# Performance work log

Measured on AMD Instinct MI355X. Metric: run time of the kernel, lower is better.

## Reference

```python
import jax, jax.numpy as jnp
import numpy as np

N = 20000   # nodes per graph batch
E = 160000  # edges
G = 128     # graphs in batch
F = 114     # node feature dim (num_features == num_features_xd)
H = 10      # GAT heads
HF = F * H  # 1140


def setup_inputs() -> dict:
    key = jax.random.key(0)
    ks = jax.random.split(key, 64)
    ki = iter(range(64))
    def rn(shape, scale=0.05):
        return jax.random.normal(ks[next(ki)], shape, dtype=jnp.float32) * scale
    inp = {}
    inp["x1"] = jax.random.normal(ks[next(ki)], (N, F), dtype=jnp.float32)
    inp["edge_index1"] = jax.random.randint(ks[next(ki)], (2, E), 0, N)
    inp["batch1"] = jnp.sort(jax.random.randint(ks[next(ki)], (N,), 0, G))
    inp["x2"] = jax.random.normal(ks[next(ki)], (N, F), dtype=jnp.float32)
    inp["edge_index2"] = jax.random.randint(ks[next(ki)], (2, E), 0, N)
    inp["batch2"] = jnp.sort(jax.random.randint(ks[next(ki)], (N,), 0, G))
    inp["target"] = jax.random.normal(ks[next(ki)], (G, 1000), dtype=jnp.float32)
    for p in ("p1", "p2"):
        inp[p + "_gatW"] = rn((F, HF))
        inp[p + "_att_src"] = rn((H, F))
        inp[p + "_att_dst"] = rn((H, F))
        inp[p + "_gatb"] = rn((HF,))
        inp[p + "_gcnW"] = rn((HF, HF))
        inp[p + "_gcnb"] = rn((HF,))
        inp[p + "_fcg1W"] = rn((2 * HF, 1000))
        inp[p + "_fcg1b"] = rn((1000,))
        inp[p + "_fcg2W"] = rn((1000, 64))
        inp[p + "_fcg2b"] = rn((64,))
    inp["fcxtW"] = rn((1000, 128)); inp["fcxtb"] = rn((128,))
    inp["fc1W"] = rn((256, 128)); inp["fc1b"] = rn((128,))
    inp["fc2W"] = rn((128, 32)); inp["fc2b"] = rn((32,))
    inp["outW"] = rn((32, 1)); inp["outb"] = rn((1,))
    return inp


def lrelu(v):
    return jax.nn.leaky_relu(v, 0.01)  # nn.LeakyReLU default slope


def gat_conv(x, src, dst, W, att_src, att_dst, b):
    # PyG GATConv (concat heads, add_self_loops handled by caller)
    h = (x @ W).reshape(N, H, F)                     # [N,H,F]
    a_s = jnp.sum(h * att_src[None], axis=-1)        # [N,H]
    a_d = jnp.sum(h * att_dst[None], axis=-1)        # [N,H]
    e = jax.nn.leaky_relu(a_s[src] + a_d[dst], 0.2)  # [E',H]
    m = jax.ops.segment_max(e, dst, num_segments=N)
    ex = jnp.exp(e - m[dst])
    den = jax.ops.segment_sum(ex, dst, num_segments=N)
    alpha = ex / den[dst]                            # softmax over incoming edges
    out = jax.ops.segment_sum(alpha[:, :, None] * h[src], dst, num_segments=N)
    return out.reshape(N, HF) + b


def gcn_conv(x, src, dst, W, b):
    # PyG GCNConv with self loops (added by caller), symmetric normalization
    deg = jax.ops.segment_sum(jnp.ones_like(dst, dtype=x.dtype), dst, num_segments=N)
    dinv = jax.lax.rsqrt(jnp.maximum(deg, 1.0))
    h = x @ W                                        # [N,HF]
    msg = (dinv[src] * dinv[dst])[:, None] * h[src]
    return jax.ops.segment_sum(msg, dst, num_segments=N) + b


def branch(x, edge_index, batch, gatW, a_s, a_d, gatb, gcnW, gcnb, f1W, f1b, f2W, f2b):
    loop = jnp.arange(N, dtype=edge_index.dtype)
    src = jnp.concatenate([edge_index[0], loop])
    dst = jnp.concatenate([edge_index[1], loop])
    h = lrelu(gat_conv(x, src, dst, gatW, a_s, a_d, gatb))
    h = lrelu(gcn_conv(h, src, dst, gcnW, gcnb))
    mx = jax.ops.segment_max(h, batch, num_segments=G)
    mx = jnp.where(jnp.isfinite(mx), mx, 0.0)        # guard empty graphs
    cnt = jax.ops.segment_sum(jnp.ones((N,), h.dtype), batch, num_segments=G)
    mean = jax.ops.segment_sum(h, batch, num_segments=G) / jnp.maximum(cnt, 1.0)[:, None]
    g = jnp.concatenate([mx, mean], axis=1)          # [G, 2*HF]
    g = lrelu(g @ f1W + f1b)                         # dropout is identity at eval
    return g @ f2W + f2b                             # [G, 64]


def reference(x1, edge_index1, batch1, x2, edge_index2, batch2, target,
              p1_gatW, p1_att_src, p1_att_dst, p1_gatb, p1_gcnW, p1_gcnb,
              p1_fcg1W, p1_fcg1b, p1_fcg2W, p1_fcg2b,
              p2_gatW, p2_att_src, p2_att_dst, p2_gatb, p2_gcnW, p2_gcnb,
              p2_fcg1W, p2_fcg1b, p2_fcg2W, p2_fcg2b,
              fcxtW, fcxtb, fc1W, fc1b, fc2W, fc2b, outW, outb):
    g1 = branch(x1, edge_index1, batch1, p1_gatW, p1_att_src, p1_att_dst, p1_gatb,
                p1_gcnW, p1_gcnb, p1_fcg1W, p1_fcg1b, p1_fcg2W, p1_fcg2b)
    g2 = branch(x2, edge_index2, batch2, p2_gatW, p2_att_src, p2_att_dst, p2_gatb,
                p2_gcnW, p2_gcnb, p2_fcg1W, p2_fcg1b, p2_fcg2W, p2_fcg2b)
    xd = jnp.concatenate([g1, g2], axis=1)           # [G,128]
    xt = target.reshape(-1, 1000) @ fcxtW + fcxtb    # [G,128]
    xc = jnp.concatenate([xd, xt], axis=1)           # [G,256]
    xc = lrelu(xc @ fc1W + fc1b)
    xc = lrelu(xc @ fc2W + fc2b)
    return xc @ outW + outb                          # [G,1]
```

## Files before the change

kernel.cpp:

```cpp
#include <hip/hip_runtime.h>
#include <cstddef>
#include <cstdint>

#define NN 20000
#define EE 160000
#define EPRIME 180000
#define GG 128
#define FF 114
#define HH 10
#define HFD 1140
#define KP 1152
#define F1K 2280
#define F1KS 18
#define F1KC 128
#define NSCB 79

typedef unsigned short ushort_t;
typedef __attribute__((ext_vector_type(8))) short bf16x8;
typedef __attribute__((ext_vector_type(4))) float f32x4;

static constexpr size_t REL  = (size_t)NN * KP;
static constexpr size_t ZREL = (size_t)10 * NN * 128;

static inline int cdiv(int a, int b) { return (a + b - 1) / b; }


__device__ __forceinline__ ushort_t f2bf(float v) {
    union { float f; unsigned u; } c; c.f = v;
    unsigned u = c.u;
    unsigned r = (u + 0x7fffu + ((u >> 16) & 1u)) >> 16;
    return (ushort_t)r;
}
__device__ __forceinline__ float bf2f(ushort_t h) {
    union { unsigned u; float f; } c; c.u = ((unsigned)h) << 16;
    return c.f;
}

__device__ __forceinline__ void gload16(const void* g, const ushort_t* l) {
    __builtin_amdgcn_global_load_lds(
        (const __attribute__((address_space(1))) unsigned int*)g,
        (__attribute__((address_space(3))) unsigned int*)l, 16, 0, 0);
}


__global__ void k_init(int* __restrict__ deg, int* __restrict__ gstart, int* __restrict__ gend) {
    int br = blockIdx.y;
    int i = blockIdx.x * blockDim.x + threadIdx.x;
    if (i < NN) deg[br * NN + i] = 1;
    if (i < GG) { gstart[br * GG + i] = NN; gend[br * GG + i] = 0; }
}

__global__ void k_count(const int* __restrict__ ei0, const int* __restrict__ ei1,
                        int* __restrict__ deg) {
    int br = blockIdx.y;
    const int* ei = br ? ei1 : ei0;
    int i = blockIdx.x * blockDim.x + threadIdx.x;
    if (i < EE) atomicAdd(&deg[br * NN + ei[EE + i]], 1);
}

__global__ void k_scan1(const int* __restrict__ deg, int* __restrict__ offs, int* __restrict__ bsum) {
    __shared__ int tmp[256];
    int br = blockIdx.y;
    deg += br * NN; offs += br * (NN + 1); bsum += br * 128;
    int b = blockIdx.x, tid = threadIdx.x;
    int i = b * 256 + tid;
    int v = (i < NN) ? deg[i] : 0;
    tmp[tid] = v;
    __syncthreads();
#pragma unroll
    for (int off = 1; off < 256; off <<= 1) {
        int t = (tid >= off) ? tmp[tid - off] : 0;
        __syncthreads();
        tmp[tid] += t;
        __syncthreads();
    }
    if (i < NN) offs[i + 1] = tmp[tid];
    if (tid == 255) bsum[b] = tmp[255];
}

__global__ void k_scan2(int* __restrict__ bsum) {
    __shared__ int tmp[128];
    bsum += blockIdx.y * 128;
    int tid = threadIdx.x;
    int v = (tid < NSCB) ? bsum[tid] : 0;
    tmp[tid] = v;
    __syncthreads();
#pragma unroll
    for (int off = 1; off < 128; off <<= 1) {
        int t = (tid >= off) ? tmp[tid - off] : 0;
        __syncthreads();
        tmp[tid] += t;
        __syncthreads();
    }
    if (tid < NSCB) bsum[tid] = tmp[tid] - v;
}

__global__ void k_scan3prep(int* __restrict__ offs, const int* __restrict__ bsum,
                            int* __restrict__ cursor, const int* __restrict__ deg,
                            float* __restrict__ dinv,
                            const int* __restrict__ batch0, const int* __restrict__ batch1,
                            int* __restrict__ gstart, int* __restrict__ gend) {
    int br = blockIdx.y;
    offs += br * (NN + 1); bsum += br * 128; cursor += br * NN;
    deg += br * NN; dinv += br * NN;
    const int* batch = br ? batch1 : batch0;
    gstart += br * GG; gend += br * GG;
    int i = blockIdx.x * 256 + threadIdx.x;
    if (i < NN) {
        int o = offs[i + 1] + bsum[i >> 8];
        offs[i + 1] = o;
        cursor[i] = o - deg[i];
        dinv[i] = rsqrtf((float)deg[i]);
        int b = batch[i];
        atomicMin(&gstart[b], i);
        atomicMax(&gend[b], i + 1);
    }
    if (i == 0) offs[0] = 0;
}

__global__ void k_fill(const int* __restrict__ ei0, const int* __restrict__ ei1,
                       int* __restrict__ cursor, int* __restrict__ csr) {
    int br = blockIdx.y;
    const int* ei = br ? ei1 : ei0;
    cursor += br * NN; csr += (size_t)br * EPRIME;
    int i = blockIdx.x * blockDim.x + threadIdx.x;
    if (i < EPRIME) {
        int s, d;
        if (i < EE) { s = ei[i]; d = ei[EE + i]; }
        else        { s = i - EE; d = s; }
        int pos = atomicAdd(&cursor[d], 1);
        csr[pos] = s;
    }
}


__global__ void k_split_x(const float* __restrict__ x0, const float* __restrict__ x1,
                          ushort_t* __restrict__ xb) {
    int br = blockIdx.y;
    const float* x = br ? x1 : x0;
    xb += (size_t)br * REL;
    int idx = blockIdx.x * 256 + threadIdx.x;
    if (idx >= NN * 128) return;
    int n = idx >> 7, k = idx & 127;
    float v = (k < FF) ? x[(size_t)n * FF + k] : 0.f;
    xb[idx] = f2bf(v);
}

__global__ __launch_bounds__(256) void k_tbf(const float* __restrict__ W0, const float* __restrict__ W1,
                                             int K, int Nc, int Kpad, ushort_t* __restrict__ T) {
    __shared__ float tile[64][65];
    int br = blockIdx.z;
    const float* W = br ? W1 : W0;
    T += (size_t)br * KP * KP;
    int kb = blockIdx.x * 64;
    int nb = blockIdx.y * 64;
    int c = threadIdx.x & 63, r4 = threadIdx.x >> 6;
#pragma unroll
    for (int rr = 0; rr < 16; ++rr) {
        int r = r4 * 16 + rr;
        int gk = kb + r, gn = nb + c;
        tile[r][c] = (gk < K && gn < Nc) ? W[(size_t)gk * Nc + gn] : 0.f;
    }
    __syncthreads();
#pragma unroll
    for (int rr = 0; rr < 16; ++rr) {
        int r = r4 * 16 + rr;
        int gn = nb + r, gk = kb + c;
        T[(size_t)gn * Kpad + gk] = f2bf(tile[c][r]);
    }
}

__global__ __launch_bounds__(256) void k_wgtT(const float* __restrict__ W0, const float* __restrict__ W1,
                                              ushort_t* __restrict__ WgT) {
    __shared__ float tile[64][65];
    int y = blockIdx.z;
    int br = y / 10, h = y - 10 * br;
    const float* W = br ? W1 : W0;
    ushort_t* T = WgT + ((size_t)br * 10 + h) * 128 * 128;
    int kb = blockIdx.x * 64, cb = blockIdx.y * 64;
    int c = threadIdx.x & 63, r4 = threadIdx.x >> 6;
#pragma unroll
    for (int rr = 0; rr < 16; ++rr) {
        int r = r4 * 16 + rr;
        int gk = kb + r, gc = cb + c;
        tile[r][c] = (gk < FF && gc < FF) ? W[(size_t)gk * HFD + h * FF + gc] : 0.f;
    }
    __syncthreads();
#pragma unroll
    for (int rr = 0; rr < 16; ++rr) {
        int r = r4 * 16 + rr;
        int gc2 = cb + r, gk2 = kb + c;
        T[(size_t)gc2 * 128 + gk2] = f2bf(tile[c][r]);
    }
}

__global__ void k_vsd(const float* __restrict__ W0, const float* __restrict__ W1,
                      const float* __restrict__ as0, const float* __restrict__ as1,
                      const float* __restrict__ ad0, const float* __restrict__ ad1,
                      float* __restrict__ Vs, float* __restrict__ Vd) {
    int br = blockIdx.y;
    const float* W = br ? W1 : W0;
    const float* asrc = br ? as1 : as0;
    const float* adst = br ? ad1 : ad0;
    int idx = blockIdx.x * 256 + threadIdx.x;
    if (idx >= 1280) return;
    int k = idx / 10, h = idx - 10 * (idx / 10);
    float vs = 0.f, vd = 0.f;
    if (k < FF) {
        const float* wrow = W + (size_t)k * HFD + h * FF;
        const float* s = asrc + h * FF;
        const float* d = adst + h * FF;
        for (int f = 0; f < FF; ++f) { vs += wrow[f] * s[f]; vd += wrow[f] * d[f]; }
    }
    Vs[br * 1280 + idx] = vs;
    Vd[br * 1280 + idx] = vd;
}

__global__ void k_att2(const ushort_t* __restrict__ xbase,
                       const float* __restrict__ Vs, const float* __restrict__ Vd,
                       float* __restrict__ as_, float* __restrict__ ad_) {
    int br = blockIdx.y;
    const ushort_t* xb = xbase + (size_t)br * REL;
    const float* vs = Vs + br * 1280;
    const float* vd = Vd + br * 1280;
    as_ += (size_t)br * NN * HH; ad_ += (size_t)br * NN * HH;
    int id = blockIdx.x * blockDim.x + threadIdx.x;
    if (id >= NN * HH) return;
    int n = id / HH, h = id - HH * (id / HH);
    const ushort_t* row = xb + (size_t)n * 128;
    float as = 0.f, ad = 0.f;
    for (int k = 0; k < FF; k += 2) {
        unsigned qq = *(const unsigned*)(row + k);
        float v0 = bf2f((ushort_t)(qq & 0xffffu));
        float v1 = bf2f((ushort_t)(qq >> 16));
        as += v0 * vs[k * 10 + h] + v1 * vs[(k + 1) * 10 + h];
        ad += v0 * vd[k * 10 + h] + v1 * vd[(k + 1) * 10 + h];
    }
    as_[id] = as;
    ad_[id] = ad;
}


template <int NU>
__device__ __forceinline__ void gax_grp(
    int eg, int end, int lane, float my_ad,
    const int* __restrict__ csr, const float* __restrict__ as_,
    const ushort_t* __restrict__ xb,
    float& den, float acc[HH][2]) {
    int s[NU]; float ex[NU];
#pragma unroll
    for (int u = 0; u < NU; ++u) {
        int idx = eg + u; if (idx > end - 1) idx = end - 1;
        s[u] = csr[idx];
    }
#pragma unroll
    for (int u = 0; u < NU; ++u) {
        float e = 0.f;
        if (lane < HH) {
            float t = as_[s[u] * HH + lane] + my_ad;
            t = (t >= 0.f) ? t : 0.2f * t;
            e = __expf(t);
            if (eg + u >= end) e = 0.f;
        }
        ex[u] = e;
        den += e;
    }
    unsigned xv[NU];
#pragma unroll
    for (int u = 0; u < NU; ++u)
        xv[u] = *(const unsigned*)(xb + (size_t)s[u] * 128 + 2 * lane);
#pragma unroll
    for (int u = 0; u < NU; ++u) {
        float x0 = bf2f((ushort_t)(xv[u] & 0xffffu));
        float x1 = bf2f((ushort_t)(xv[u] >> 16));
#pragma unroll
        for (int h = 0; h < HH; ++h) {
            float w = __shfl(ex[u], h, 64);
            acc[h][0] += w * x0;
            acc[h][1] += w * x1;
        }
    }
}

__global__ __launch_bounds__(256) void gat_aggx(
    const ushort_t* __restrict__ xbase,
    const float* __restrict__ as_, const float* __restrict__ ad_,
    const int* __restrict__ offs, const int* __restrict__ csr,
    ushort_t* __restrict__ Z) {
    int br = blockIdx.y;
    const ushort_t* xb = xbase + (size_t)br * REL;
    as_ += (size_t)br * NN * HH; ad_ += (size_t)br * NN * HH;
    offs += br * (NN + 1); csr += (size_t)br * EPRIME;
    ushort_t* Zb = Z + (size_t)br * ZREL;

    int lane = threadIdx.x & 63;
    int n = blockIdx.x * 4 + (threadIdx.x >> 6);
    if (n >= NN) return;
    int beg = offs[n], end = offs[n + 1];
    float my_ad = (lane < HH) ? ad_[n * HH + lane] : 0.f;

    float den = 0.f;
    float acc[HH][2];
#pragma unroll
    for (int h = 0; h < HH; ++h) { acc[h][0] = 0.f; acc[h][1] = 0.f; }

    int eg = beg;
    for (; eg + 8 <= end; eg += 8)
        gax_grp<8>(eg, end, lane, my_ad, csr, as_, xb, den, acc);
    for (; eg < end; eg += 4)
        gax_grp<4>(eg, end, lane, my_ad, csr, as_, xb, den, acc);

#pragma unroll
    for (int h = 0; h < HH; ++h) {
        float d = __shfl(den, h, 64);
        float inv = 1.f / d;
        unsigned pk = (unsigned)f2bf(acc[h][0] * inv)
                    | ((unsigned)f2bf(acc[h][1] * inv) << 16);
        *(unsigned*)(Zb + ((size_t)h * NN + n) * 128 + 2 * lane) = pk;
    }
}


__global__ __launch_bounds__(256) void mfma_hgemm(
    const ushort_t* __restrict__ Zbase, const ushort_t* __restrict__ WgT,
    const float* __restrict__ b0, const float* __restrict__ b1,
    ushort_t* __restrict__ Cbase) {
    __shared__ __align__(16) ushort_t lds[2 * 8192];
    int y = blockIdx.y;
    int br = y / 10, h = y - 10 * br;
    const ushort_t* A = Zbase + (size_t)br * ZREL + (size_t)h * NN * 128;
    const ushort_t* Bt = WgT + ((size_t)br * 10 + h) * 128 * 128;
    const float* bias = (br ? b1 : b0) + h * FF;
    ushort_t* Cb = Cbase + (size_t)br * REL;

    const int tid = threadIdx.x;
    const int lane = tid & 63;
    const int w = tid >> 6;
    const int wr = w >> 1, wc = w & 1;

    int nwg = gridDim.x;
    int q = nwg >> 3, r8 = nwg & 7;
    int xcd = blockIdx.x & 7, sidx = blockIdx.x >> 3;
    int wg = (xcd < r8 ? xcd * (q + 1) : r8 * (q + 1) + (xcd - r8) * q) + sidx;

    int row0 = wg * 128; if (row0 > NN - 128) row0 = NN - 128;

    f32x4 acc[4][4];
#pragma unroll
    for (int i = 0; i < 4; ++i)
#pragma unroll
        for (int j = 0; j < 4; ++j) acc[i][j] = (f32x4){0.f, 0.f, 0.f, 0.f};

    const char* pA[2]; const char* pB[2];
    unsigned ldsoff[2];
#pragma unroll
    for (int i = 0; i < 2; ++i) {
        int c = (w * 2 + i) * 64 + lane;
        int kg = c >> 7, r = c & 127;
        pA[i] = (const char*)A + (size_t)(row0 + r) * 256 + kg * 16;
        pB[i] = (const char*)Bt + (size_t)r * 256 + kg * 16;
        ldsoff[i] = (w * 2 + i) * 512;
    }
    const int kgf = lane >> 4, r15 = lane & 15;

    auto STAGE = [&](int buf, int ks) {
        size_t kb = (size_t)ks * 64;
        unsigned bo = buf ? 8192u : 0u;
#pragma unroll
        for (int i = 0; i < 2; ++i) {
            gload16(pA[i] + kb, lds + bo + 0 + ldsoff[i]);
            gload16(pB[i] + kb, lds + bo + 4096 + ldsoff[i]);
        }
    };

    STAGE(0, 0);
    asm volatile("s_waitcnt vmcnt(0)" ::: "memory");
    __syncthreads();
    int cur = 0;

    for (int ks = 0; ks < 4; ++ks) {
        if (ks + 1 < 4) STAGE(cur ^ 1, ks + 1);
        const ushort_t* lb = lds + (cur ? 8192u : 0u);
        bf16x8 ah[4], bh[4];
#pragma unroll
        for (int i = 0; i < 4; ++i) {
            int ra = wr * 64 + i * 16 + r15;
            int rb = wc * 64 + i * 16 + r15;
            ah[i] = *(const bf16x8*)(lb + 0 + kgf * 1024 + ra * 8);
            bh[i] = *(const bf16x8*)(lb + 4096 + kgf * 1024 + rb * 8);
        }
#pragma unroll
        for (int i = 0; i < 4; ++i)
#pragma unroll
            for (int j = 0; j < 4; ++j)
                acc[i][j] = __builtin_amdgcn_mfma_f32_16x16x32_bf16(ah[i], bh[j], acc[i][j], 0, 0, 0);
        asm volatile("s_waitcnt vmcnt(0)" ::: "memory");
        __syncthreads();
        cur ^= 1;
    }

    const int g4 = lane >> 4;
#pragma unroll
    for (int i = 0; i < 4; ++i)
#pragma unroll
        for (int j = 0; j < 4; ++j) {
            int c = wc * 64 + j * 16 + r15;
#pragma unroll
            for (int reg = 0; reg < 4; ++reg) {
                int r = row0 + wr * 64 + i * 16 + g4 * 4 + reg;
                int gc = h * FF + c;
                if (c < FF) {
                    float v = acc[i][j][reg] + bias[c];
                    v = (v >= 0.f) ? v : 0.01f * v;
                    Cb[(size_t)r * KP + gc] = f2bf(v);
                } else if (h == 9 && gc < KP) {
                    Cb[(size_t)r * KP + gc] = 0;
                }
            }
        }
}


__global__ __launch_bounds__(256) void mfma_gemm(
    const ushort_t* __restrict__ Abase, const ushort_t* __restrict__ Btbase,
    int lda, int ldb, int M, int Nreal, int ksteps, int ncb,
    ushort_t* __restrict__ Cbase, int ldcs) {
    __shared__ __align__(16) ushort_t lds[2 * 8192];
    const int br = blockIdx.y;
    const ushort_t* A = Abase + (size_t)br * REL;
    const ushort_t* Bt = Btbase + (size_t)br * KP * KP;
    ushort_t* Cb = Cbase + (size_t)br * ZREL;

    const int tid = threadIdx.x;
    const int lane = tid & 63;
    const int w = tid >> 6;
    const int wr = w >> 1, wc = w & 1;

    int nwg = gridDim.x;
    int q = nwg >> 3, r8 = nwg & 7;
    int xcd = blockIdx.x & 7, sidx = blockIdx.x >> 3;
    int wg = (xcd < r8 ? xcd * (q + 1) : r8 * (q + 1) + (xcd - r8) * q) + sidx;
    int brow = wg / ncb, bcol = wg - brow * ncb;

    int row0 = brow * 128; if (row0 > M - 128) row0 = M - 128;
    const int col0 = bcol * 128;

    f32x4 acc[4][4];
#pragma unroll
    for (int i = 0; i < 4; ++i)
#pragma unroll
        for (int j = 0; j < 4; ++j) acc[i][j] = (f32x4){0.f, 0.f, 0.f, 0.f};

    const size_t ldaB = (size_t)lda * 2, ldbB = (size_t)ldb * 2;
    const char* pA[2]; const char* pB[2];
    unsigned ldsoff[2];
#pragma unroll
    for (int i = 0; i < 2; ++i) {
        int c = (w * 2 + i) * 64 + lane;
        int kg = c >> 7, r = c & 127;
        pA[i] = (const char*)A + (size_t)(row0 + r) * ldaB + kg * 16;
        pB[i] = (const char*)Bt + (size_t)(col0 + r) * ldbB + kg * 16;
        ldsoff[i] = (w * 2 + i) * 512;
    }
    const int kgf = lane >> 4, r15 = lane & 15;

    auto STAGE = [&](int buf, int ks) {
        size_t kb = (size_t)ks * 64;
        unsigned bo = buf ? 8192u : 0u;
#pragma unroll
        for (int i = 0; i < 2; ++i) {
            gload16(pA[i] + kb, lds + bo + 0 + ldsoff[i]);
            gload16(pB[i] + kb, lds + bo + 4096 + ldsoff[i]);
        }
    };

    STAGE(0, 0);
    asm volatile("s_waitcnt vmcnt(0)" ::: "memory");
    __syncthreads();
    int cur = 0;

    for (int ks = 0; ks < ksteps; ++ks) {
        if (ks + 1 < ksteps) STAGE(cur ^ 1, ks + 1);
        const ushort_t* lb = lds + (cur ? 8192u : 0u);
        bf16x8 ah[4], bh[4];
#pragma unroll
        for (int i = 0; i < 4; ++i) {
            int ra = wr * 64 + i * 16 + r15;
            int rb = wc * 64 + i * 16 + r15;
            ah[i] = *(const bf16x8*)(lb + 0 + kgf * 1024 + ra * 8);
            bh[i] = *(const bf16x8*)(lb + 4096 + kgf * 1024 + rb * 8);
        }
#pragma unroll
        for (int i = 0; i < 4; ++i)
#pragma unroll
            for (int j = 0; j < 4; ++j)
                acc[i][j] = __builtin_amdgcn_mfma_f32_16x16x32_bf16(ah[i], bh[j], acc[i][j], 0, 0, 0);
        asm volatile("s_waitcnt vmcnt(0)" ::: "memory");
        __syncthreads();
        cur ^= 1;
    }

    const int g4 = lane >> 4;
#pragma unroll
    for (int i = 0; i < 4; ++i)
#pragma unroll
        for (int j = 0; j < 4; ++j) {
            int c = col0 + wc * 64 + j * 16 + r15;
#pragma unroll
            for (int reg = 0; reg < 4; ++reg) {
                int r = row0 + wr * 64 + i * 16 + g4 * 4 + reg;
                if (r < M) {
                    float v = (c < Nreal) ? acc[i][j][reg] : 0.f;
                    Cb[(size_t)r * ldcs + c] = f2bf(v);
                }
            }
        }
}


template <int NU, int HASB>
__device__ __forceinline__ void gcn_grp(
    int eg, int end, int lane, float di,
    const int* __restrict__ csr, const float* __restrict__ dinv,
    const ushort_t* __restrict__ h2b, int kbA, int kbB,
    float* accA, float* accB) {
    int s[NU]; float w[NU];
#pragma unroll
    for (int u = 0; u < NU; ++u) {
        int idx = eg + u; if (idx > end - 1) idx = end - 1;
        s[u] = csr[idx];
    }
#pragma unroll
    for (int u = 0; u < NU; ++u) {
        float ww = dinv[s[u]] * di;
        w[u] = (eg + u < end) ? ww : 0.f;
    }
    bf16x8 qv[NU];
#pragma unroll
    for (int u = 0; u < NU; ++u) qv[u] = *(const bf16x8*)(h2b + (size_t)s[u] * KP + kbA);
#pragma unroll
    for (int u = 0; u < NU; ++u)
#pragma unroll
        for (int e = 0; e < 8; ++e) accA[e] += w[u] * bf2f((ushort_t)qv[u][e]);
    if (HASB && lane < 16) {
#pragma unroll
        for (int u = 0; u < NU; ++u) qv[u] = *(const bf16x8*)(h2b + (size_t)s[u] * KP + kbB);
#pragma unroll
        for (int u = 0; u < NU; ++u)
#pragma unroll
            for (int e = 0; e < 8; ++e) accB[e] += w[u] * bf2f((ushort_t)qv[u][e]);
    }
}

__global__ __launch_bounds__(256) void gcn_agg(
    const ushort_t* __restrict__ h2base, const int* __restrict__ offs, const int* __restrict__ csr,
    const float* __restrict__ dinv,
    const float* __restrict__ b0, const float* __restrict__ b1,
    ushort_t* __restrict__ outbase) {
    int br = blockIdx.y;
    const ushort_t* h2b = h2base + (size_t)br * ZREL;
    offs += br * (NN + 1); csr += (size_t)br * EPRIME; dinv += br * NN;
    const float* bias = br ? b1 : b0;
    ushort_t* outb = outbase + (size_t)br * REL;

    int lane = threadIdx.x & 63;
    int wid = threadIdx.x >> 6;
    int n = blockIdx.x * 2 + (wid >> 1);
    int half = wid & 1;
    if (n >= NN) return;
    int beg = offs[n], end = offs[n + 1];
    float di = dinv[n];
    const int kbA = (half ? 512 : 0) + 8 * lane;
    const int kbB = 1024 + 8 * lane;
    float accA[8] = {}, accB[8] = {};

    int eg = beg;
    if (half == 0) {
        for (; eg + 8 <= end; eg += 8)
            gcn_grp<8, 1>(eg, end, lane, di, csr, dinv, h2b, kbA, kbB, accA, accB);
        for (; eg < end; eg += 4)
            gcn_grp<4, 1>(eg, end, lane, di, csr, dinv, h2b, kbA, kbB, accA, accB);
    } else {
        for (; eg + 8 <= end; eg += 8)
            gcn_grp<8, 0>(eg, end, lane, di, csr, dinv, h2b, kbA, kbB, accA, accB);
        for (; eg < end; eg += 4)
            gcn_grp<4, 0>(eg, end, lane, di, csr, dinv, h2b, kbA, kbB, accA, accB);
    }

    {
        bf16x8 vb;
#pragma unroll
        for (int e = 0; e < 8; ++e) {
            float v = accA[e] + bias[kbA + e];
            v = (v >= 0.f) ? v : 0.01f * v;
            vb[e] = (short)f2bf(v);
        }
        *(bf16x8*)(outb + (size_t)n * KP + kbA) = vb;
    }
    if (half == 0 && lane < 16) {
        bf16x8 vb;
#pragma unroll
        for (int e = 0; e < 8; ++e) {
            int k = kbB + e;
            float v = 0.f;
            if (k < HFD) {
                v = accB[e] + bias[k];
                v = (v >= 0.f) ? v : 0.01f * v;
            }
            vb[e] = (short)f2bf(v);
        }
        *(bf16x8*)(outb + (size_t)n * KP + kbB) = vb;
    }
}


__global__ void k_pool(const ushort_t* __restrict__ hbase, const int* __restrict__ gs,
                       const int* __restrict__ ge, float* __restrict__ gpool) {
    int br = blockIdx.z;
    const ushort_t* hfeat = hbase + (size_t)br * REL;
    gs += br * GG; ge += br * GG;
    float* gout = gpool + (size_t)br * GG * 2 * HFD;
    if (threadIdx.x >= 48) return;
    int g = blockIdx.x;
    int mg = blockIdx.y * 48 + threadIdx.x;
    int s = gs[g], e = ge[g];
    int cnt = e - s;
    float mx[8], sm[8];
#pragma unroll
    for (int j = 0; j < 8; ++j) { mx[j] = -1e30f; sm[j] = 0.f; }
    for (int r = s; r < e; ++r) {
        bf16x8 qv = *(const bf16x8*)(hfeat + (size_t)r * KP + 8 * mg);
#pragma unroll
        for (int j = 0; j < 8; ++j) {
            float v = bf2f((ushort_t)qv[j]);
            mx[j] = fmaxf(mx[j], v);
            sm[j] += v;
        }
    }
    float inv = (cnt > 0) ? 1.f / (float)cnt : 0.f;
#pragma unroll
    for (int j = 0; j < 8; ++j) {
        int k = 8 * mg + j;
        if (k < HFD) {
            float m = (cnt > 0) ? mx[j] : 0.f;
            gout[(size_t)g * (2 * HFD) + k] = m;
            gout[(size_t)g * (2 * HFD) + HFD + k] = sm[j] * inv;
        }
    }
}


__global__ __launch_bounds__(256) void k_fcg1_part(
    const float* __restrict__ gpool, const float* __restrict__ B0, const float* __restrict__ B1,
    float* __restrict__ p0, float* __restrict__ p1) {
    __shared__ float As[16][64 + 4];
    __shared__ float Bs[16][64 + 4];
    int br = blockIdx.y >> 1, rowblk = blockIdx.y & 1;
    const float* A = gpool + (size_t)br * GG * F1K;
    const float* B = br ? B1 : B0;
    float* part = br ? p1 : p0;
    int tid = threadIdx.x;
    int tx = tid & 15, ty = tid >> 4;
    int row0 = rowblk * 64, col0 = blockIdx.x * 64;
    int kbeg = blockIdx.z * F1KC;
    float acc[4][4] = {};
#pragma unroll 1
    for (int kt = 0; kt < F1KC / 16; ++kt) {
        int kk = kbeg + kt * 16;
#pragma unroll
        for (int l = 0; l < 4; ++l) {
            int idx = tid + 256 * l;
            int m = idx >> 4, k = idx & 15;
            int gr = row0 + m, gk = kk + k;
            As[k][m] = (gk < F1K) ? A[(size_t)gr * F1K + gk] : 0.f;
        }
#pragma unroll
        for (int l = 0; l < 4; ++l) {
            int idx = tid + 256 * l;
            int nn = idx & 63, k = idx >> 6;
            int gc = col0 + nn, gk = kk + k;
            Bs[k][nn] = (gc < 1000 && gk < F1K) ? B[(size_t)gk * 1000 + gc] : 0.f;
        }
        __syncthreads();
#pragma unroll
        for (int k = 0; k < 16; ++k) {
            float4 av = *(const float4*)&As[k][ty * 4];
            float4 bv = *(const float4*)&Bs[k][tx * 4];
            float a[4] = {av.x, av.y, av.z, av.w};
            float b[4] = {bv.x, bv.y, bv.z, bv.w};
#pragma unroll
            for (int i = 0; i < 4; ++i)
#pragma unroll
                for (int j = 0; j < 4; ++j) acc[i][j] += a[i] * b[j];
        }
        __syncthreads();
    }
    float* pc = part + (size_t)blockIdx.z * GG * 1000;
#pragma unroll
    for (int i = 0; i < 4; ++i) {
        int r = row0 + ty * 4 + i;
#pragma unroll
        for (int j = 0; j < 4; ++j) {
            int c = col0 + tx * 4 + j;
            if (c < 1000) pc[(size_t)r * 1000 + c] = acc[i][j];
        }
    }
}

__global__ void k_fcg1_red(const float* __restrict__ p0, const float* __restrict__ p1,
                           const float* __restrict__ b0, const float* __restrict__ b1,
                           float* __restrict__ fc1out) {
    int br = blockIdx.y;
    const float* part = br ? p1 : p0;
    const float* bias = br ? b1 : b0;
    float* out = fc1out + (size_t)br * GG * 1000;
    int idx = blockIdx.x * 256 + threadIdx.x;
    if (idx >= GG * 1000) return;
    float s = 0.f;
#pragma unroll
    for (int k = 0; k < F1KS; ++k) s += part[(size_t)k * GG * 1000 + idx];
    int n = idx % 1000;
    float v = s + bias[n];
    out[idx] = (v >= 0.f) ? v : 0.01f * v;
}


__global__ __launch_bounds__(256) void k_fcg2(const float* __restrict__ fc1out,
                                              const float* __restrict__ W0, const float* __restrict__ W1,
                                              const float* __restrict__ b0, const float* __restrict__ b1,
                                              float* __restrict__ bout) {
    __shared__ float part[4][64];
    int br = blockIdx.y;
    const float* in = fc1out + (size_t)br * GG * 1000;
    const float* W = br ? W1 : W0;
    const float* b = br ? b1 : b0;
    float* out = bout + (size_t)br * GG * 64;
    int g = blockIdx.x;
    int o = threadIdx.x & 63, p = threadIdx.x >> 6;
    const float* row = in + (size_t)g * 1000;
    float acc = 0.f;
    for (int k = p * 250; k < (p + 1) * 250; ++k) acc += row[k] * W[k * 64 + o];
    part[p][o] = acc;
    __syncthreads();
    if (p == 0) out[(size_t)g * 64 + o] = part[0][o] + part[1][o] + part[2][o] + part[3][o] + b[o];
}


__global__ __launch_bounds__(256) void k_final(
    const float* __restrict__ b1, const float* __restrict__ b2, const float* __restrict__ target,
    const float* __restrict__ fcxtW, const float* __restrict__ fcxtb,
    const float* __restrict__ fc1W, const float* __restrict__ fc1b,
    const float* __restrict__ fc2W, const float* __restrict__ fc2b,
    const float* __restrict__ outW, const float* __restrict__ outb,
    float* __restrict__ out) {
    __shared__ float xc[256];
    __shared__ float xt2[128];
    __shared__ float y1[128];
    __shared__ float y2[32];
    int g = blockIdx.x, t = threadIdx.x;
    if (t < 64) xc[t] = b1[(size_t)g * 64 + t];
    else if (t < 128) xc[t] = b2[(size_t)g * 64 + (t - 64)];
    {
        int c = t & 127, p = t >> 7;
        float acc = 0.f;
        const float* trow = target + (size_t)g * 1000;
        for (int k = p * 500; k < (p + 1) * 500; ++k) acc += trow[k] * fcxtW[k * 128 + c];
        if (p == 1) xt2[c] = acc;
        __syncthreads();
        if (p == 0) xc[128 + c] = acc + xt2[c] + fcxtb[c];
    }
    __syncthreads();
    if (t < 128) {
        float acc = 0.f;
        for (int k = 0; k < 256; ++k) acc += xc[k] * fc1W[k * 128 + t];
        acc += fc1b[t];
        y1[t] = (acc >= 0.f) ? acc : 0.01f * acc;
    }
    __syncthreads();
    if (t < 32) {
        float acc = 0.f;
        for (int k = 0; k < 128; ++k) acc += y1[k] * fc2W[k * 32 + t];
        acc += fc2b[t];
        y2[t] = (acc >= 0.f) ? acc : 0.01f * acc;
    }
    __syncthreads();
    if (t == 0) {
        float acc = 0.f;
        for (int k = 0; k < 32; ++k) acc += y2[k] * outW[k];
        out[g] = acc + outb[0];
    }
}


extern "C" void kernel_launch(void* const* d_in, const int* in_sizes, int n_in,
                              void* d_out, int out_size, void* d_ws, size_t ws_size,
                              hipStream_t stream) {
    (void)in_sizes; (void)n_in; (void)out_size; (void)ws_size;

    size_t off = 0;
    auto alloc = [&](size_t bytes) -> void* {
        void* p = (char*)d_ws + off;
        off += (bytes + 255) & ~(size_t)255;
        return p;
    };
    char* brA = (char*)alloc(2 * ZREL * 2);
    char* brB = (char*)alloc(2 * REL * 2);
    ushort_t* Bt  = (ushort_t*)alloc(2 * (size_t)KP * KP * 2);
    ushort_t* WgT = (ushort_t*)alloc(20 * (size_t)128 * 128 * 2);
    float* Vs     = (float*)alloc(2 * 1280 * 4);
    float* Vd     = (float*)alloc(2 * 1280 * 4);
    float* a_s    = (float*)alloc(2 * (size_t)NN * HH * 4);
    float* a_d    = (float*)alloc(2 * (size_t)NN * HH * 4);
    int*   deg    = (int*)alloc(2 * (size_t)NN * 4);
    int*   offs   = (int*)alloc(2 * (size_t)(NN + 1) * 4);
    int*   cursor = (int*)alloc(2 * (size_t)NN * 4);
    int*   csr    = (int*)alloc(2 * (size_t)EPRIME * 4);
    float* dinv   = (float*)alloc(2 * (size_t)NN * 4);
    int*   gstart = (int*)alloc(2 * (size_t)GG * 4);
    int*   gend   = (int*)alloc(2 * (size_t)GG * 4);
    int*   bsum   = (int*)alloc(2 * (size_t)128 * 4);
    float* gpool  = (float*)alloc(2 * (size_t)GG * 2 * HFD * 4);
    float* fc1out = (float*)alloc(2 * (size_t)GG * 1000 * 4);
    float* bout   = (float*)alloc(2 * (size_t)GG * 64 * 4);

    ushort_t* Zb  = (ushort_t*)brA;
    float* f1p0 = (float*)brA;
    float* f1p1 = (float*)(brA + (size_t)F1KS * GG * 1000 * 4);
    ushort_t* xb  = (ushort_t*)brB;

    const float* target = (const float*)d_in[6];
    const int NRB = cdiv(NN, 128);
    const int NCB = KP / 128;

    const float* x0 = (const float*)d_in[0];
    const float* x1 = (const float*)d_in[3];
    const int* ei0 = (const int*)d_in[1];
    const int* ei1 = (const int*)d_in[4];
    const int* batch0 = (const int*)d_in[2];
    const int* batch1 = (const int*)d_in[5];
    const float *gatW0 = (const float*)d_in[7],  *gatW1 = (const float*)d_in[17];
    const float *asrc0 = (const float*)d_in[8],  *asrc1 = (const float*)d_in[18];
    const float *adst0 = (const float*)d_in[9],  *adst1 = (const float*)d_in[19];
    const float *gatb0 = (const float*)d_in[10], *gatb1 = (const float*)d_in[20];
    const float *gcnW0 = (const float*)d_in[11], *gcnW1 = (const float*)d_in[21];
    const float *gcnb0 = (const float*)d_in[12], *gcnb1 = (const float*)d_in[22];
    const float *f1W0  = (const float*)d_in[13], *f1W1  = (const float*)d_in[23];
    const float *f1b0  = (const float*)d_in[14], *f1b1  = (const float*)d_in[24];
    const float *f2W0  = (const float*)d_in[15], *f2W1  = (const float*)d_in[25];
    const float *f2b0  = (const float*)d_in[16], *f2b1  = (const float*)d_in[26];

    hipLaunchKernelGGL(k_init, dim3(cdiv(NN, 256), 2), dim3(256), 0, stream, deg, gstart, gend);
    hipLaunchKernelGGL(k_count, dim3(cdiv(EE, 256), 2), dim3(256), 0, stream, ei0, ei1, deg);
    hipLaunchKernelGGL(k_scan1, dim3(NSCB, 2), dim3(256), 0, stream, deg, offs, bsum);
    hipLaunchKernelGGL(k_scan2, dim3(1, 2), dim3(128), 0, stream, bsum);
    hipLaunchKernelGGL(k_scan3prep, dim3(NSCB, 2), dim3(256), 0, stream,
                       offs, bsum, cursor, deg, dinv, batch0, batch1, gstart, gend);
    hipLaunchKernelGGL(k_fill, dim3(cdiv(EPRIME, 256), 2), dim3(256), 0, stream, ei0, ei1, cursor, csr);

    hipLaunchKernelGGL(k_split_x, dim3(cdiv(NN * 128, 256), 2), dim3(256), 0, stream, x0, x1, xb);
    hipLaunchKernelGGL(k_wgtT, dim3(2, 2, 20), dim3(256), 0, stream, gatW0, gatW1, WgT);
    hipLaunchKernelGGL(k_vsd, dim3(5, 2), dim3(256), 0, stream,
                       gatW0, gatW1, asrc0, asrc1, adst0, adst1, Vs, Vd);

    hipLaunchKernelGGL(k_att2, dim3(cdiv(NN * HH, 256), 2), dim3(256), 0, stream,
                       xb, Vs, Vd, a_s, a_d);

    hipLaunchKernelGGL(gat_aggx, dim3(cdiv(NN, 4), 2), dim3(256), 0, stream,
                       xb, a_s, a_d, offs, csr, Zb);

    hipLaunchKernelGGL(mfma_hgemm, dim3(NRB, 20), dim3(256), 0, stream,
                       Zb, WgT, gatb0, gatb1, xb);

    hipLaunchKernelGGL(k_tbf, dim3(KP / 64, KP / 64, 2), dim3(256), 0, stream,
                       gcnW0, gcnW1, HFD, HFD, KP, Bt);

    hipLaunchKernelGGL(mfma_gemm, dim3(NRB * NCB, 2), dim3(256), 0, stream,
                       xb, Bt, KP, KP, NN, HFD, KP / 32, NCB, Zb, KP);

    hipLaunchKernelGGL(gcn_agg, dim3(cdiv(NN, 2), 2), dim3(256), 0, stream,
                       Zb, offs, csr, dinv, gcnb0, gcnb1, xb);

    hipLaunchKernelGGL(k_pool, dim3(GG, 3, 2), dim3(64), 0, stream, xb, gstart, gend, gpool);

    hipLaunchKernelGGL(k_fcg1_part, dim3(16, 4, F1KS), dim3(256), 0, stream,
                       gpool, f1W0, f1W1, f1p0, f1p1);
    hipLaunchKernelGGL(k_fcg1_red, dim3(cdiv(GG * 1000, 256), 2), dim3(256), 0, stream,
                       f1p0, f1p1, f1b0, f1b1, fc1out);

    hipLaunchKernelGGL(k_fcg2, dim3(GG, 2), dim3(256), 0, stream,
                       fc1out, f2W0, f2W1, f2b0, f2b1, bout);

    hipLaunchKernelGGL(k_final, dim3(GG), dim3(256), 0, stream,
                       bout, bout + (size_t)GG * 64, target,
                       (const float*)d_in[27], (const float*)d_in[28],
                       (const float*)d_in[29], (const float*)d_in[30],
                       (const float*)d_in[31], (const float*)d_in[32],
                       (const float*)d_in[33], (const float*)d_in[34],
                       (float*)d_out);
}
```

Before: 847.8 us.

## Load GEMM B fragments directly to registers and rebalance GCN aggregation per node

In the MFMA GEMM, the B tile is no longer staged through shared memory. Each wave loads its own B fragments straight from global memory into registers, with the next step's fragments prefetched, which halves LDS use per block. The GCN aggregation now gives each node a full 256-thread block in which 4 waves each cover 36 of the 144 feature groups, replacing the uneven split where one half-wave pair also handled the tail columns. The trade-offs are redundant global reads of B across waves sharing a column tile, and 28 idle lanes per wave in the aggregation kernel.

```diff
diff --git a/kernel.cpp b/kernel.cpp
--- a/kernel.cpp
+++ b/kernel.cpp
@@ -425,7 +425,7 @@
     const ushort_t* __restrict__ Abase, const ushort_t* __restrict__ Btbase,
     int lda, int ldb, int M, int Nreal, int ksteps, int ncb,
     ushort_t* __restrict__ Cbase, int ldcs) {
-    __shared__ __align__(16) ushort_t lds[2 * 8192];
+    __shared__ __align__(16) ushort_t lds[2 * 4096];
     const int br = blockIdx.y;
     const ushort_t* A = Abase + (size_t)br * REL;
     const ushort_t* Bt = Btbase + (size_t)br * KP * KP;
@@ -451,52 +451,67 @@
 #pragma unroll
         for (int j = 0; j < 4; ++j) acc[i][j] = (f32x4){0.f, 0.f, 0.f, 0.f};
 
-    const size_t ldaB = (size_t)lda * 2, ldbB = (size_t)ldb * 2;
-    const char* pA[2]; const char* pB[2];
-    unsigned ldsoff[2];
+    const size_t ldaB = (size_t)lda * 2;
+    const char* pA[2];
+    unsigned ldst[2];
 #pragma unroll
     for (int i = 0; i < 2; ++i) {
-        int c = (w * 2 + i) * 64 + lane;
+        int c = i * 256 + tid;
         int kg = c >> 7, r = c & 127;
         pA[i] = (const char*)A + (size_t)(row0 + r) * ldaB + kg * 16;
-        pB[i] = (const char*)Bt + (size_t)(col0 + r) * ldbB + kg * 16;
-        ldsoff[i] = (w * 2 + i) * 512;
+        ldst[i] = (unsigned)c * 8;
     }
     const int kgf = lane >> 4, r15 = lane & 15;
 
-    auto STAGE = [&](int buf, int ks) {
+    const ushort_t* bp0 = Bt + (size_t)(col0 + wc * 64 + 0 * 16 + r15) * ldb + kgf * 8;
+    const ushort_t* bp1 = Bt + (size_t)(col0 + wc * 64 + 1 * 16 + r15) * ldb + kgf * 8;
+    const ushort_t* bp2 = Bt + (size_t)(col0 + wc * 64 + 2 * 16 + r15) * ldb + kgf * 8;
+    const ushort_t* bp3 = Bt + (size_t)(col0 + wc * 64 + 3 * 16 + r15) * ldb + kgf * 8;
+
+    auto STAGE_A = [&](int buf, int ks) {
         size_t kb = (size_t)ks * 64;
-        unsigned bo = buf ? 8192u : 0u;
-#pragma unroll
-        for (int i = 0; i < 2; ++i) {
-            gload16(pA[i] + kb, lds + bo + 0 + ldsoff[i]);
-            gload16(pB[i] + kb, lds + bo + 4096 + ldsoff[i]);
-        }
+        unsigned bo = buf ? 4096u : 0u;
+#pragma unroll
+        for (int i = 0; i < 2; ++i)
+            gload16(pA[i] + kb, lds + bo + ldst[i]);
     };
 
-    STAGE(0, 0);
+    STAGE_A(0, 0);
+    bf16x8 bc0 = *(const bf16x8*)(bp0);
+    bf16x8 bc1 = *(const bf16x8*)(bp1);
+    bf16x8 bc2 = *(const bf16x8*)(bp2);
+    bf16x8 bc3 = *(const bf16x8*)(bp3);
     asm volatile("s_waitcnt vmcnt(0)" ::: "memory");
     __syncthreads();
     int cur = 0;
 
     for (int ks = 0; ks < ksteps; ++ks) {
-        if (ks + 1 < ksteps) STAGE(cur ^ 1, ks + 1);
-        const ushort_t* lb = lds + (cur ? 8192u : 0u);
-        bf16x8 ah[4], bh[4];
+        bf16x8 bn0, bn1, bn2, bn3;
+        if (ks + 1 < ksteps) {
+            int ko = (ks + 1) * 32;
+            STAGE_A(cur ^ 1, ks + 1);
+            bn0 = *(const bf16x8*)(bp0 + ko);
+            bn1 = *(const bf16x8*)(bp1 + ko);
+            bn2 = *(const bf16x8*)(bp2 + ko);
+            bn3 = *(const bf16x8*)(bp3 + ko);
+        }
+        const ushort_t* lb = lds + (cur ? 4096u : 0u);
+        bf16x8 ah[4];
 #pragma unroll
         for (int i = 0; i < 4; ++i) {
             int ra = wr * 64 + i * 16 + r15;
-            int rb = wc * 64 + i * 16 + r15;
-            ah[i] = *(const bf16x8*)(lb + 0 + kgf * 1024 + ra * 8);
-            bh[i] = *(const bf16x8*)(lb + 4096 + kgf * 1024 + rb * 8);
-        }
-#pragma unroll
-        for (int i = 0; i < 4; ++i)
-#pragma unroll
-            for (int j = 0; j < 4; ++j)
-                acc[i][j] = __builtin_amdgcn_mfma_f32_16x16x32_bf16(ah[i], bh[j], acc[i][j], 0, 0, 0);
+            ah[i] = *(const bf16x8*)(lb + kgf * 1024 + ra * 8);
+        }
+#pragma unroll
+        for (int i = 0; i < 4; ++i) {
+            acc[i][0] = __builtin_amdgcn_mfma_f32_16x16x32_bf16(ah[i], bc0, acc[i][0], 0, 0, 0);
+            acc[i][1] = __builtin_amdgcn_mfma_f32_16x16x32_bf16(ah[i], bc1, acc[i][1], 0, 0, 0);
+            acc[i][2] = __builtin_amdgcn_mfma_f32_16x16x32_bf16(ah[i], bc2, acc[i][2], 0, 0, 0);
+            acc[i][3] = __builtin_amdgcn_mfma_f32_16x16x32_bf16(ah[i], bc3, acc[i][3], 0, 0, 0);
+        }
         asm volatile("s_waitcnt vmcnt(0)" ::: "memory");
         __syncthreads();
+        if (ks + 1 < ksteps) { bc0 = bn0; bc1 = bn1; bc2 = bn2; bc3 = bn3; }
         cur ^= 1;
     }
 
@@ -518,12 +533,11 @@
 }
 
 
-template <int NU, int HASB>
+template <int NU>
 __device__ __forceinline__ void gcn_grp(
-    int eg, int end, int lane, float di,
+    int eg, int end, bool act, float di,
     const int* __restrict__ csr, const float* __restrict__ dinv,
-    const ushort_t* __restrict__ h2b, int kbA, int kbB,
-    float* accA, float* accB) {
+    const ushort_t* __restrict__ h2b, int kb, float* acc) {
     int s[NU]; float w[NU];
 #pragma unroll
     for (int u = 0; u < NU; ++u) {
@@ -535,20 +549,14 @@
         float ww = dinv[s[u]] * di;
         w[u] = (eg + u < end) ? ww : 0.f;
     }
-    bf16x8 qv[NU];
-#pragma unroll
-    for (int u = 0; u < NU; ++u) qv[u] = *(const bf16x8*)(h2b + (size_t)s[u] * KP + kbA);
-#pragma unroll
-    for (int u = 0; u < NU; ++u)
-#pragma unroll
-        for (int e = 0; e < 8; ++e) accA[e] += w[u] * bf2f((ushort_t)qv[u][e]);
-    if (HASB && lane < 16) {
-#pragma unroll
-        for (int u = 0; u < NU; ++u) qv[u] = *(const bf16x8*)(h2b + (size_t)s[u] * KP + kbB);
+    if (act) {
+        bf16x8 qv[NU];
+#pragma unroll
+        for (int u = 0; u < NU; ++u) qv[u] = *(const bf16x8*)(h2b + (size_t)s[u] * KP + kb);
 #pragma unroll
         for (int u = 0; u < NU; ++u)
 #pragma unroll
-            for (int e = 0; e < 8; ++e) accB[e] += w[u] * bf2f((ushort_t)qv[u][e]);
+            for (int e = 0; e < 8; ++e) acc[e] += w[u] * bf2f((ushort_t)qv[u][e]);
     }
 }
 
@@ -564,52 +572,34 @@
     ushort_t* outb = outbase + (size_t)br * REL;
 
     int lane = threadIdx.x & 63;
-    int wid = threadIdx.x >> 6;
-    int n = blockIdx.x * 2 + (wid >> 1);
-    int half = wid & 1;
-    if (n >= NN) return;
+    int qw = threadIdx.x >> 6;
+    int n = blockIdx.x;
+    int g = qw * 36 + lane;
+    bool act = lane < 36;
+    const int kb = g * 8;
     int beg = offs[n], end = offs[n + 1];
     float di = dinv[n];
-    const int kbA = (half ? 512 : 0) + 8 * lane;
-    const int kbB = 1024 + 8 * lane;
-    float accA[8] = {}, accB[8] = {};
+    float acc[8] = {};
 
     int eg = beg;
-    if (half == 0) {
-        for (; eg + 8 <= end; eg += 8)
-            gcn_grp<8, 1>(eg, end, lane, di, csr, dinv, h2b, kbA, kbB, accA, accB);
-        for (; eg < end; eg += 4)
-            gcn_grp<4, 1>(eg, end, lane, di, csr, dinv, h2b, kbA, kbB, accA, accB);
-    } else {
-        for (; eg + 8 <= end; eg += 8)
-            gcn_grp<8, 0>(eg, end, lane, di, csr, dinv, h2b, kbA, kbB, accA, accB);
-        for (; eg < end; eg += 4)
-            gcn_grp<4, 0>(eg, end, lane, di, csr, dinv, h2b, kbA, kbB, accA, accB);
-    }
-
-    {
+    for (; eg + 8 <= end; eg += 8)
+        gcn_grp<8>(eg, end, act, di, csr, dinv, h2b, kb, acc);
+    for (; eg < end; eg += 4)
+        gcn_grp<4>(eg, end, act, di, csr, dinv, h2b, kb, acc);
+
+    if (act) {
         bf16x8 vb;
 #pragma unroll
         for (int e = 0; e < 8; ++e) {
-            float v = accA[e] + bias[kbA + e];
-            v = (v >= 0.f) ? v : 0.01f * v;
-            vb[e] = (short)f2bf(v);
-        }
-        *(bf16x8*)(outb + (size_t)n * KP + kbA) = vb;
-    }
-    if (half == 0 && lane < 16) {
-        bf16x8 vb;
-#pragma unroll
-        for (int e = 0; e < 8; ++e) {
-            int k = kbB + e;
+            int k = kb + e;
             float v = 0.f;
             if (k < HFD) {
-                v = accB[e] + bias[k];
+                v = acc[e] + bias[k];
                 v = (v >= 0.f) ? v : 0.01f * v;
             }
             vb[e] = (short)f2bf(v);
         }
-        *(bf16x8*)(outb + (size_t)n * KP + kbB) = vb;
+        *(bf16x8*)(outb + (size_t)n * KP + kb) = vb;
     }
 }
 
@@ -877,7 +867,7 @@
     hipLaunchKernelGGL(mfma_gemm, dim3(NRB * NCB, 2), dim3(256), 0, stream,
                        xb, Bt, KP, KP, NN, HFD, KP / 32, NCB, Zb, KP);
 
-    hipLaunchKernelGGL(gcn_agg, dim3(cdiv(NN, 2), 2), dim3(256), 0, stream,
+    hipLaunchKernelGGL(gcn_agg, dim3(NN, 2), dim3(256), 0, stream,
                        Zb, offs, csr, dinv, gcnb0, gcnb1, xb);
 
     hipLaunchKernelGGL(k_pool, dim3(GG, 3, 2), dim3(64), 0, stream, xb, gstart, gend, gpool);
```

Result: slower. 953.1 us (+12.4%).
